# Performance work log

Hardware: AMD Instinct MI355X
Metric: run time of the kernel (lower is better)

Reference implementation:

```python
import jax, jax.numpy as jnp
import numpy as np

DIM = 2048      # model dim
H = 32          # num_heads
N = 128         # state_dim
G = 1           # num_groups
K = 4           # conv_size
HID = 4096     # hidden_dim = multiple_of*ceil(2.0*DIM/256)
P = HID // H    # head_dim = 128
CHUNK = 256
EPS = 1e-6
DT_MIN, DT_MAX = 0.001, 0.1


def setup_inputs() -> dict:
    key = jax.random.key(0)
    ks = jax.random.split(key, 8)
    b, s = 2, 2048
    d_in = 2 * HID + 2 * G * N + H           # 8448
    conv_dim = HID + 2 * G * N               # 4352
    return {
        "x": jax.random.normal(ks[0], (b, s, DIM), jnp.float32),
        "W_in": jax.random.normal(ks[1], (d_in, DIM), jnp.float32) / np.sqrt(DIM),
        "conv_w": jax.random.normal(ks[2], (conv_dim, K), jnp.float32) / np.sqrt(K),
        "conv_b": jnp.zeros((conv_dim,), jnp.float32),
        "dt_bias": jnp.zeros((H,), jnp.float32),
        "A_log": jnp.log(jax.random.uniform(ks[3], (H,), jnp.float32, 1.0, 16.0)),
        "D": jnp.ones((H,), jnp.float32),
        "norm_w": jnp.ones((HID,), jnp.float32),
        "W_out": jax.random.normal(ks[4], (DIM, HID), jnp.float32) / np.sqrt(HID),
    }


def _causal_conv_silu(xBC, w, bias):
    # depthwise causal conv1d, kernel K, then SiLU. xBC: (b,s,c), w: (c,K)
    b, s, c = xBC.shape
    xp = jnp.pad(xBC, ((0, 0), (K - 1, 0), (0, 0)))
    y = sum(xp[:, k:k + s, :] * w[:, k] for k in range(K)) + bias
    return jax.nn.silu(y)


def _chunked_scan(x, dt, A, B, C, D):
    # Mamba2 chunked selective scan.
    # x:(b,s,h,p) dt:(b,s,h) A:(h,) B,C:(b,s,n) (groups=1) D:(h,)
    b, s, h, p = x.shape
    n = B.shape[-1]
    nc, L = s // CHUNK, CHUNK
    xc = x.reshape(b, nc, L, h, p)
    dtc = dt.reshape(b, nc, L, h)
    Bc = B.reshape(b, nc, L, n)
    Cc = C.reshape(b, nc, L, n)

    dA = dtc * A                          # (b,nc,L,h), A<0
    dA_cs = jnp.cumsum(dA, axis=2)        # (b,nc,L,h)

    # intra-chunk contribution
    seg = dA_cs[:, :, :, None, :] - dA_cs[:, :, None, :, :]   # (b,nc,L,L,h)
    mask = jnp.tril(jnp.ones((L, L), bool))[None, None, :, :, None]
    decay = jnp.exp(jnp.where(mask, seg, -jnp.inf))
    CB = jnp.einsum('bcln,bcsn->bcls', Cc, Bc)                # (b,nc,L,L)
    y_intra = jnp.einsum('bcls,bclsh,bcsh,bcshp->bclhp', CB, decay, dtc, xc)

    # per-chunk final states
    decay_states = jnp.exp(dA_cs[:, :, -1:, :] - dA_cs)       # (b,nc,L,h)
    states = jnp.einsum('bclh,bclh,bclhp,bcln->bchpn', decay_states, dtc, xc, Bc)

    # inter-chunk recurrence over chunk index
    dA_chunk = dA_cs[:, :, -1, :]                              # (b,nc,h)
    def step(prev, inp):
        st, dec = inp
        new = prev * jnp.exp(dec)[:, :, None, None] + st
        return new, prev
    init = jnp.zeros((b, h, p, n), x.dtype)
    _, prev_states = jax.lax.scan(step, init,
                                  (jnp.moveaxis(states, 1, 0), jnp.moveaxis(dA_chunk, 1, 0)))
    prev_states = jnp.moveaxis(prev_states, 0, 1)              # state at start of each chunk

    y_inter = jnp.einsum('bcln,bclh,bchpn->bclhp', Cc, jnp.exp(dA_cs), prev_states)
    y = (y_intra + y_inter).reshape(b, s, h, p)
    return y + x * D[None, None, :, None]


def reference(x, W_in, conv_w, conv_b, dt_bias, A_log, D, norm_w, W_out):
    b, s, _ = x.shape
    zxbcdt = x @ W_in.T                                        # (b,s,2*HID+2GN+H)
    z, xBC, dt = jnp.split(zxbcdt, [HID, 2 * HID + 2 * G * N], axis=-1)
    xBC = _causal_conv_silu(xBC, conv_w, conv_b)
    xs, B, C = jnp.split(xBC, [HID, HID + G * N], axis=-1)
    A = -jnp.exp(A_log)
    dt = jnp.clip(jax.nn.softplus(dt + dt_bias), DT_MIN, DT_MAX)
    xs = xs.reshape(b, s, H, P)
    y = _chunked_scan(xs, dt, A, B, C, D).reshape(b, s, HID)
    y = y * jax.nn.silu(z)                                     # gate, norm_before_gate=False
    y = y * jax.lax.rsqrt(jnp.mean(y * y, axis=-1, keepdims=True) + EPS) * norm_w
    return y @ W_out.T
```

## Files before the change

### kernel.cpp

```cpp
#include <hip/hip_runtime.h>


typedef short s16x8 __attribute__((ext_vector_type(8)));
typedef float f32x4 __attribute__((ext_vector_type(4)));

__device__ __forceinline__ float bf2f(ushort u) {
    return __builtin_bit_cast(float, (unsigned)u << 16);
}
__device__ __forceinline__ ushort f2bf(float f) {
    unsigned u = __builtin_bit_cast(unsigned, f);
    unsigned r = u + 0x7fffu + ((u >> 16) & 1u);
    return (ushort)(r >> 16);
}

__device__ __forceinline__ void gld16(const void* g, void* l) {
    __builtin_amdgcn_global_load_lds((__attribute__((address_space(1))) void*)g,
                                     (__attribute__((address_space(3))) void*)l, 16, 0, 0);
}

#define BARRIER() asm volatile("s_barrier" ::: "memory")

__global__ void cast_all_k(const float4* __restrict__ x, const float4* __restrict__ wout,
                           const float4* __restrict__ win, ushort* __restrict__ xb,
                           ushort* __restrict__ woutb, ushort* __restrict__ winb) {
    const long b = blockIdx.x, tid = threadIdx.x;
    if (b < 8192) {
        long i = b * 256 + tid;
        float4 v = x[i];
        ushort4 o = { f2bf(v.x), f2bf(v.y), f2bf(v.z), f2bf(v.w) };
        *(ushort4*)(xb + i * 4) = o;
    } else if (b < 16384) {
        long i = (b - 8192) * 256 + tid;
        float4 v = wout[i];
        ushort4 o = { f2bf(v.x), f2bf(v.y), f2bf(v.z), f2bf(v.w) };
        *(ushort4*)(woutb + i * 4) = o;
    } else {
        long i = (b - 16384) * 256 + tid;
        ushort4 o;
        if (i < 4341760L) {
            float4 v = win[i];
            o = { f2bf(v.x), f2bf(v.y), f2bf(v.z), f2bf(v.w) };
        } else {
            o = { 0, 0, 0, 0 };
        }
        *(ushort4*)(winb + i * 4) = o;
    }
}

__global__ __launch_bounds__(512) void gemm1_k(const ushort* __restrict__ A,
                                               const ushort* __restrict__ Bm,
                                               ushort* __restrict__ zbuf,
                                               ushort* __restrict__ xbc,
                                               ushort* __restrict__ dtr) {
    constexpr int K = 2048, NT = 64;
    __shared__ ushort lds[2 * 8192 + 2 * 6144];
    const int tid = threadIdx.x, lane = tid & 63, wave = tid >> 6;
    const int wm = wave >> 2, wn = wave & 3;
    const int bid = blockIdx.x;
    const int xcd = bid & 7, w = bid >> 3;
    const int mt = xcd * 2 + (w & 1), nt = w >> 1;
    const long m0 = (long)mt * 256, n0 = (long)nt * 192;

    const int st_row = lane >> 2;
    const int st_gc = ((lane & 3) * 8) ^ (((lane >> 5) & 1) << 4);

    auto STAGE = [&](int buf, int kt) {
#pragma unroll
        for (int j = 0; j < 2; j++) {
            int sidx = wave + j * 8;
            gld16(A + (m0 + sidx * 16 + st_row) * K + kt + st_gc,
                  lds + buf * 8192 + sidx * 512 + lane * 8);
        }
#pragma unroll
        for (int j = 0; j < 2; j++) {
            int sidx = wave + j * 8;
            if (sidx < 12)
                gld16(Bm + (n0 + sidx * 16 + st_row) * K + kt + st_gc,
                      lds + 16384 + buf * 6144 + sidx * 512 + lane * 8);
        }
    };

    const int cfr = (lane >> 4) * 8;
    const int lr = lane & 15;
    auto LDFA = [&](int buf, int r) -> s16x8 {
        int off = buf * 8192 + ((r >> 4) << 9) + ((r & 15) << 5)
                + (cfr ^ (((r >> 3) & 1) << 4));
        return *(const s16x8*)(lds + off);
    };
    auto LDFB = [&](int buf, int r) -> s16x8 {
        int off = 16384 + buf * 6144 + ((r >> 4) << 9) + ((r & 15) << 5)
                + (cfr ^ (((r >> 3) & 1) << 4));
        return *(const s16x8*)(lds + off);
    };

    f32x4 zero = { 0.f, 0.f, 0.f, 0.f };
    f32x4 acc[8][3];
#pragma unroll
    for (int i = 0; i < 8; i++)
#pragma unroll
        for (int j = 0; j < 3; j++) acc[i][j] = zero;

    STAGE(0, 0);
    asm volatile("s_waitcnt vmcnt(0)" ::: "memory");
    BARRIER();

    for (int t = 0; t < NT; ++t) {
        const int cur = t & 1;
        if ((t + 1) < NT) STAGE((t + 1) & 1, (t + 1) * 32);

        s16x8 bfr[3], alo[4], ahi[4];
#pragma unroll
        for (int ni = 0; ni < 3; ni++) bfr[ni] = LDFB(cur, wn * 48 + ni * 16 + lr);
#pragma unroll
        for (int mi = 0; mi < 4; mi++) alo[mi] = LDFA(cur, wm * 128 + mi * 16 + lr);
#pragma unroll
        for (int mi = 0; mi < 4; mi++) ahi[mi] = LDFA(cur, wm * 128 + 64 + mi * 16 + lr);

        __builtin_amdgcn_s_setprio(1);
#pragma unroll
        for (int mi = 0; mi < 4; mi++)
#pragma unroll
            for (int ni = 0; ni < 3; ni++)
                acc[mi][ni] = __builtin_amdgcn_mfma_f32_16x16x32_bf16(alo[mi], bfr[ni], acc[mi][ni], 0, 0, 0);
#pragma unroll
        for (int mi = 0; mi < 4; mi++)
#pragma unroll
            for (int ni = 0; ni < 3; ni++)
                acc[mi + 4][ni] = __builtin_amdgcn_mfma_f32_16x16x32_bf16(ahi[mi], bfr[ni], acc[mi + 4][ni], 0, 0, 0);
        __builtin_amdgcn_s_setprio(0);

        asm volatile("s_waitcnt vmcnt(0)" ::: "memory");
        BARRIER();
    }

    const int lr4 = (lane >> 4) * 4;
#pragma unroll
    for (int mi = 0; mi < 8; mi++) {
#pragma unroll
        for (int ni = 0; ni < 3; ni++) {
            const long col = n0 + wn * 48 + ni * 16 + lr;
            ushort* dst;
            long stride;
            if (col < 4096)      { dst = zbuf + col;         stride = 4096; }
            else if (col < 8448) { dst = xbc + (col - 4096); stride = 4352; }
            else if (col < 8480) { dst = dtr + (col - 8448); stride = 32;   }
            else continue;
            const long row0 = m0 + wm * 128 + mi * 16 + lr4;
#pragma unroll
            for (int r = 0; r < 4; r++) dst[(row0 + r) * stride] = f2bf(acc[mi][ni][r]);
        }
    }
}

__global__ __launch_bounds__(256) void gemm2_k(const ushort* __restrict__ A,
                                               const ushort* __restrict__ Bm,
                                               float* __restrict__ Cout) {
    constexpr int K = 4096, NT = 128;
    __shared__ ushort lds[2 * 4096 + 2 * 4096];
    const int tid = threadIdx.x, lane = tid & 63, wave = tid >> 6;
    const int wm = wave >> 1, wn = wave & 1;
    const int bid = blockIdx.x;
    const int xcd = bid & 7, w = bid >> 3;
    const int mt = xcd * 4 + (w & 3), nt = w >> 2;
    const long m0 = (long)mt * 128, n0 = (long)nt * 128;

    const int st_row = lane >> 2;
    const int st_gc = ((lane & 3) * 8) ^ (((lane >> 5) & 1) << 4);

    auto STAGE = [&](int buf, int kt) {
#pragma unroll
        for (int j = 0; j < 2; j++) {
            int sidx = wave + j * 4;
            gld16(A + (m0 + sidx * 16 + st_row) * K + kt + st_gc,
                  lds + buf * 4096 + sidx * 512 + lane * 8);
        }
#pragma unroll
        for (int j = 0; j < 2; j++) {
            int sidx = wave + j * 4;
            gld16(Bm + (n0 + sidx * 16 + st_row) * K + kt + st_gc,
                  lds + 8192 + buf * 4096 + sidx * 512 + lane * 8);
        }
    };

    const int cfr = (lane >> 4) * 8;
    const int lr = lane & 15;
    auto LDFA = [&](int buf, int r) -> s16x8 {
        int off = buf * 4096 + ((r >> 4) << 9) + ((r & 15) << 5)
                + (cfr ^ (((r >> 3) & 1) << 4));
        return *(const s16x8*)(lds + off);
    };
    auto LDFB = [&](int buf, int r) -> s16x8 {
        int off = 8192 + buf * 4096 + ((r >> 4) << 9) + ((r & 15) << 5)
                + (cfr ^ (((r >> 3) & 1) << 4));
        return *(const s16x8*)(lds + off);
    };

    f32x4 zero = { 0.f, 0.f, 0.f, 0.f };
    f32x4 acc[4][4];
#pragma unroll
    for (int i = 0; i < 4; i++)
#pragma unroll
        for (int j = 0; j < 4; j++) acc[i][j] = zero;

    STAGE(0, 0);
    asm volatile("s_waitcnt vmcnt(0)" ::: "memory");
    BARRIER();

    for (int t = 0; t < NT; ++t) {
        const int cur = t & 1;
        if ((t + 1) < NT) STAGE((t + 1) & 1, (t + 1) * 32);

        s16x8 af[4], bf[4];
#pragma unroll
        for (int mi = 0; mi < 4; mi++) af[mi] = LDFA(cur, wm * 64 + mi * 16 + lr);
#pragma unroll
        for (int ni = 0; ni < 4; ni++) bf[ni] = LDFB(cur, wn * 64 + ni * 16 + lr);

        __builtin_amdgcn_s_setprio(1);
#pragma unroll
        for (int mi = 0; mi < 4; mi++)
#pragma unroll
            for (int ni = 0; ni < 4; ni++)
                acc[mi][ni] = __builtin_amdgcn_mfma_f32_16x16x32_bf16(af[mi], bf[ni], acc[mi][ni], 0, 0, 0);
        __builtin_amdgcn_s_setprio(0);

        asm volatile("s_waitcnt vmcnt(0)" ::: "memory");
        BARRIER();
    }

    const long crow = m0 + wm * 64 + ((lane >> 4) << 2);
    const long ccol = n0 + wn * 64 + (lane & 15);
#pragma unroll
    for (int mi = 0; mi < 4; mi++)
#pragma unroll
        for (int ni = 0; ni < 4; ni++)
#pragma unroll
            for (int r = 0; r < 4; r++)
                Cout[(crow + mi * 16 + r) * 2048 + ccol + ni * 16] = acc[mi][ni][r];
}

__global__ __launch_bounds__(256) void convx_k(const ushort* __restrict__ xbc,
                                               const float* __restrict__ w,
                                               const float* __restrict__ bias,
                                               ushort* __restrict__ xbcc,
                                               ushort* __restrict__ xT,
                                               ushort* __restrict__ Bt) {
    __shared__ ushort xin[35][136];
    __shared__ ushort yL[32][132];
    const int stile = blockIdx.x, slot = blockIdx.y, bc = blockIdx.z;
    const int tid = threadIdx.x;
    const int cc = bc & 7;
    const long tbase = (long)bc * 256 + stile * 32;
    const int c0 = slot * 128;
    const bool head = (cc == 0 && stile == 0);

#pragma unroll
    for (int i = 0; i < 3; i++) {
        int u = tid + i * 256;
        if (u < 560) {
            int r = u >> 4, seg = u & 15;
            s16x8 v;
            if (head && r < 3) {
#pragma unroll
                for (int j = 0; j < 8; j++) v[j] = 0;
            } else {
                v = *(const s16x8*)&xbc[(tbase - 3 + r) * 4352 + c0 + seg * 8];
            }
            *(s16x8*)&xin[r][seg * 8] = v;
        }
    }
    __syncthreads();

    const int s_loc = tid >> 3, p0 = (tid & 7) * 16;
    ushort yo[16];
#pragma unroll
    for (int j = 0; j < 16; j++) {
        int c = p0 + j;
        float a = bias[c0 + c];
#pragma unroll
        for (int k = 0; k < 4; k++)
            a += bf2f(xin[s_loc + k][c]) * w[(c0 + c) * 4 + k];
        float yv = a / (1.f + __expf(-a));
        ushort ub = f2bf(yv);
        yo[j] = ub;
        yL[s_loc][c] = ub;
    }
    *(s16x8*)&xbcc[(tbase + s_loc) * 4352 + c0 + p0] = *(const s16x8*)&yo[0];
    *(s16x8*)&xbcc[(tbase + s_loc) * 4352 + c0 + p0 + 8] = *(const s16x8*)&yo[8];
    __syncthreads();

    if (slot < 33) {
        const int p = tid >> 1, s0 = (tid & 1) * 16;
        ushort o[16];
#pragma unroll
        for (int j = 0; j < 16; j++) o[j] = yL[s0 + j][p];
        ushort* dst = (slot < 32)
            ? (xT + ((long)(bc * 32 + slot) * 128 + p) * 256 + stile * 32 + s0)
            : (Bt + ((long)bc * 128 + p) * 256 + stile * 32 + s0);
        *(s16x8*)&dst[0] = *(const s16x8*)&o[0];
        *(s16x8*)&dst[8] = *(const s16x8*)&o[8];
    }
}

__global__ void prep_k(const ushort* __restrict__ dtr, const float* __restrict__ dt_bias,
                       const float* __restrict__ A_log, float* __restrict__ dtp,
                       float* __restrict__ dacs) {
    const int bx = blockIdx.x;
    const int h = bx & 31, cc = (bx >> 5) & 7, bi = bx >> 8;
    const int lane = threadIdx.x;
    const float A = -__expf(A_log[h]);
    const float bsh = dt_bias[h];
    float v[4], cs[4];
    float run = 0.f;
#pragma unroll
    for (int j = 0; j < 4; j++) {
        int pos = cc * 256 + lane * 4 + j;
        float raw = bf2f(dtr[((long)(bi * 2048 + pos)) * 32 + h]) + bsh;
        float sp = (raw > 20.f) ? raw : log1pf(__expf(raw));
        float d = fminf(fmaxf(sp, 0.001f), 0.1f);
        v[j] = d;
        run += d * A;
        cs[j] = run;
    }
    float tot = run, pre = run;
    for (int off = 1; off < 64; off <<= 1) {
        float u = __shfl_up(pre, off, 64);
        if (lane >= off) pre += u;
    }
    float excl = pre - tot;
    const long base = ((long)(bi * 32 + h)) * 2048 + cc * 256 + lane * 4;
#pragma unroll
    for (int j = 0; j < 4; j++) { dtp[base + j] = v[j]; dacs[base + j] = excl + cs[j]; }
}

__global__ __launch_bounds__(256) void cb_mfma_k(const ushort* __restrict__ xbcc,
                                                 float* __restrict__ CB) {
    const int bid = blockIdx.x;
    const int sq = bid & 1, lq = (bid >> 1) & 1, bc = bid >> 2;
    const int tid = threadIdx.x, lane = tid & 63, wave = tid >> 6;
    const int wm = wave >> 1, wn = wave & 1;
    const long tbase = (long)bc * 256;

    f32x4 zero = { 0.f, 0.f, 0.f, 0.f };
    f32x4 acc[4][4];
#pragma unroll
    for (int i = 0; i < 4; i++)
#pragma unroll
        for (int j = 0; j < 4; j++) acc[i][j] = zero;

    for (int kst = 0; kst < 4; ++kst) {
        const int koff = kst * 32 + (lane >> 4) * 8;
        s16x8 a[4], b[4];
#pragma unroll
        for (int mi = 0; mi < 4; mi++) {
            int l = lq * 128 + wm * 64 + mi * 16 + (lane & 15);
            a[mi] = *(const s16x8*)&xbcc[(tbase + l) * 4352 + 4224 + koff];
        }
#pragma unroll
        for (int ni = 0; ni < 4; ni++) {
            int s = sq * 128 + wn * 64 + ni * 16 + (lane & 15);
            b[ni] = *(const s16x8*)&xbcc[(tbase + s) * 4352 + 4096 + koff];
        }
#pragma unroll
        for (int mi = 0; mi < 4; mi++)
#pragma unroll
            for (int ni = 0; ni < 4; ni++)
                acc[mi][ni] = __builtin_amdgcn_mfma_f32_16x16x32_bf16(a[mi], b[ni], acc[mi][ni], 0, 0, 0);
    }

    float* out = CB + (long)bc * 65536;
#pragma unroll
    for (int mi = 0; mi < 4; mi++)
#pragma unroll
        for (int ni = 0; ni < 4; ni++)
#pragma unroll
            for (int r = 0; r < 4; r++) {
                int l = lq * 128 + wm * 64 + mi * 16 + (lane >> 4) * 4 + r;
                int s = sq * 128 + wn * 64 + ni * 16 + (lane & 15);
                out[(long)l * 256 + s] = acc[mi][ni][r];
            }
}

__global__ __launch_bounds__(256) void scan_mfma_k(const ushort* __restrict__ xT,
                                                   const float* __restrict__ CB,
                                                   const float* __restrict__ dtp,
                                                   const float* __restrict__ dacs,
                                                   const ushort* __restrict__ xbcc,
                                                   const float* __restrict__ st,
                                                   float* __restrict__ yf) {
    const int bx = blockIdx.x;
    const int ltile = bx & 1, h = (bx >> 1) & 31, cc = (bx >> 6) & 7, bi = bx >> 9;
    const int tid = threadIdx.x, lane = tid & 63, wave = tid >> 6;
    const int wm = wave >> 1, wn = wave & 1;

    __shared__ float dA_s[256];
    __shared__ float F_s[256];

    const long dbase = ((long)(bi * 32 + h)) * 2048 + cc * 256;
    {
        float a = dacs[dbase + tid];
        float r = dacs[dbase + (tid | 31)];
        dA_s[tid] = a;
        F_s[tid] = __expf(r - a) * dtp[dbase + tid];
    }
    __syncthreads();

    int lch[4];
    float dAl[4];
#pragma unroll
    for (int mi = 0; mi < 4; mi++) {
        lch[mi] = ltile * 128 + wm * 64 + mi * 16 + (lane & 15);
        dAl[mi] = dA_s[lch[mi]];
    }

    f32x4 zero = { 0.f, 0.f, 0.f, 0.f };
    f32x4 acc[4][4];
#pragma unroll
    for (int i = 0; i < 4; i++)
#pragma unroll
        for (int j = 0; j < 4; j++) acc[i][j] = zero;

    const long tbase = (long)bi * 2048 + cc * 256;
    const long cbbase = ((long)(bi * 8 + cc)) * 65536;
    const ushort* xrow = xT + (((long)(bi * 8 + cc) * 32 + h) * 128) * 256;
    const int nsb = ltile * 4 + 4;

    for (int sb = 0; sb < nsb; ++sb) {
        const int soff = sb * 32 + (lane >> 4) * 8;
        s16x8 bf[4];
#pragma unroll
        for (int ni = 0; ni < 4; ni++) {
            int p = wn * 64 + ni * 16 + (lane & 15);
            bf[ni] = *(const s16x8*)&xrow[(long)p * 256 + soff];
        }
        const float Rsb = dA_s[sb * 32 + 31];
        const int s0 = soff;
#pragma unroll
        for (int mi = 0; mi < 4; mi++) {
            const int lb = lch[mi] >> 5;
            if (sb > lb) continue;
            const float* cbrow = CB + cbbase + (long)lch[mi] * 256 + s0;
            float4 c0 = *(const float4*)cbrow;
            float4 c1 = *(const float4*)(cbrow + 4);
            float E = __expf(dAl[mi] - Rsb);
            float m[8];
            m[0] = c0.x * E * F_s[s0 + 0]; m[1] = c0.y * E * F_s[s0 + 1];
            m[2] = c0.z * E * F_s[s0 + 2]; m[3] = c0.w * E * F_s[s0 + 3];
            m[4] = c1.x * E * F_s[s0 + 4]; m[5] = c1.y * E * F_s[s0 + 5];
            m[6] = c1.z * E * F_s[s0 + 6]; m[7] = c1.w * E * F_s[s0 + 7];
            if (sb == lb) {
#pragma unroll
                for (int j = 0; j < 8; j++)
                    if (s0 + j > lch[mi]) m[j] = 0.f;
            }
            s16x8 a;
#pragma unroll
            for (int j = 0; j < 8; j++) a[j] = (short)f2bf(m[j]);
#pragma unroll
            for (int ni = 0; ni < 4; ni++)
                acc[mi][ni] = __builtin_amdgcn_mfma_f32_16x16x32_bf16(a, bf[ni], acc[mi][ni], 0, 0, 0);
        }
    }

    const float* sbase = st + (((long)(bi * 8 + cc) * 32 + h) * 128) * 128;
    float eAr[4];
#pragma unroll
    for (int mi = 0; mi < 4; mi++) eAr[mi] = __expf(dAl[mi]);
    for (int kk = 0; kk < 4; ++kk) {
        const int koff = kk * 32 + (lane >> 4) * 8;
        s16x8 a[4], b[4];
#pragma unroll
        for (int mi = 0; mi < 4; mi++) {
            s16x8 raw = *(const s16x8*)&xbcc[(tbase + lch[mi]) * 4352 + 4224 + koff];
#pragma unroll
            for (int j = 0; j < 8; j++)
                a[mi][j] = (short)f2bf(bf2f((ushort)raw[j]) * eAr[mi]);
        }
#pragma unroll
        for (int ni = 0; ni < 4; ni++) {
            int p = wn * 64 + ni * 16 + (lane & 15);
            const float* pr = sbase + (long)p * 128 + koff;
            float4 v0 = *(const float4*)pr;
            float4 v1 = *(const float4*)(pr + 4);
            b[ni][0] = (short)f2bf(v0.x); b[ni][1] = (short)f2bf(v0.y);
            b[ni][2] = (short)f2bf(v0.z); b[ni][3] = (short)f2bf(v0.w);
            b[ni][4] = (short)f2bf(v1.x); b[ni][5] = (short)f2bf(v1.y);
            b[ni][6] = (short)f2bf(v1.z); b[ni][7] = (short)f2bf(v1.w);
        }
#pragma unroll
        for (int mi = 0; mi < 4; mi++)
#pragma unroll
            for (int ni = 0; ni < 4; ni++)
                acc[mi][ni] = __builtin_amdgcn_mfma_f32_16x16x32_bf16(a[mi], b[ni], acc[mi][ni], 0, 0, 0);
    }

    const long crow = tbase + ltile * 128 + wm * 64 + ((lane >> 4) << 2);
    const int ccol = h * 128 + wn * 64 + (lane & 15);
#pragma unroll
    for (int mi = 0; mi < 4; mi++)
#pragma unroll
        for (int ni = 0; ni < 4; ni++)
#pragma unroll
            for (int r = 0; r < 4; r++)
                yf[(crow + mi * 16 + r) * 4096 + ccol + ni * 16] = acc[mi][ni][r];
}

__global__ __launch_bounds__(256) void states_mfma_k(const ushort* __restrict__ xT,
                                                     const ushort* __restrict__ Bt,
                                                     const float* __restrict__ dtp,
                                                     const float* __restrict__ dacs,
                                                     float* __restrict__ states) {
    const int bx = blockIdx.x;
    const int h = bx & 31, cc = (bx >> 5) & 7, bi = bx >> 8;
    const int bc = bi * 8 + cc;
    const int tid = threadIdx.x, lane = tid & 63, wave = tid >> 6;
    const int wm = wave >> 1, wn = wave & 1;
    __shared__ float wl[256];
    const long dbase = ((long)(bi * 32 + h)) * 2048 + cc * 256;
    {
        float last = dacs[dbase + 255];
        wl[tid] = __expf(last - dacs[dbase + tid]) * dtp[dbase + tid];
    }
    __syncthreads();

    f32x4 zero = { 0.f, 0.f, 0.f, 0.f };
    f32x4 acc[4][4];
#pragma unroll
    for (int i = 0; i < 4; i++)
#pragma unroll
        for (int j = 0; j < 4; j++) acc[i][j] = zero;

    const ushort* xrow = xT + (((long)bc * 32 + h) * 128) * 256;
    const ushort* brow = Bt + ((long)bc * 128) * 256;

    for (int sb = 0; sb < 8; ++sb) {
        const int soff = sb * 32 + (lane >> 4) * 8;
        s16x8 a[4], b[4];
#pragma unroll
        for (int mi = 0; mi < 4; mi++) {
            int p = wm * 64 + mi * 16 + (lane & 15);
            s16x8 raw = *(const s16x8*)&xrow[(long)p * 256 + soff];
#pragma unroll
            for (int j = 0; j < 8; j++)
                a[mi][j] = (short)f2bf(bf2f((ushort)raw[j]) * wl[soff + j]);
        }
#pragma unroll
        for (int ni = 0; ni < 4; ni++) {
            int n = wn * 64 + ni * 16 + (lane & 15);
            b[ni] = *(const s16x8*)&brow[(long)n * 256 + soff];
        }
#pragma unroll
        for (int mi = 0; mi < 4; mi++)
#pragma unroll
            for (int ni = 0; ni < 4; ni++)
                acc[mi][ni] = __builtin_amdgcn_mfma_f32_16x16x32_bf16(a[mi], b[ni], acc[mi][ni], 0, 0, 0);
    }

    float* out = states + (((long)bc * 32 + h) * 128) * 128;
#pragma unroll
    for (int mi = 0; mi < 4; mi++)
#pragma unroll
        for (int ni = 0; ni < 4; ni++)
#pragma unroll
            for (int r = 0; r < 4; r++) {
                int p = wm * 64 + mi * 16 + (lane >> 4) * 4 + r;
                int n = wn * 64 + ni * 16 + (lane & 15);
                out[(long)p * 128 + n] = acc[mi][ni][r];
            }
}

__global__ void rec_k(float* __restrict__ states, const float* __restrict__ dacs) {
    const int i = blockIdx.x * 256 + threadIdx.x;
    const int n = i & 127, p = (i >> 7) & 127, h = (i >> 14) & 31, bi = i >> 19;
    const long dbase = ((long)(bi * 32 + h)) * 2048;
    float run = 0.f;
    for (int cc = 0; cc < 8; cc++) {
        const long off = ((((long)(bi * 8 + cc)) * 32 + h) * 128 + p) * 128 + n;
        float st = states[off];
        states[off] = run;
        float dec = dacs[dbase + cc * 256 + 255];
        run = run * __expf(dec) + st;
    }
}

__global__ __launch_bounds__(256) void gate_rms_k(const float* __restrict__ y, const ushort* __restrict__ zbuf,
                                                  const ushort* __restrict__ xbcc, const float* __restrict__ Dv,
                                                  const float* __restrict__ norm_w, ushort* __restrict__ yb) {
    const int t = blockIdx.x, tid = threadIdx.x;
    const float* yr = &y[(long)t * 4096];
    const ushort* zr = &zbuf[(long)t * 4096];
    const ushort* xr = &xbcc[(long)t * 4352];
    float g[16];
    float ss = 0.f;
#pragma unroll
    for (int j = 0; j < 16; j++) {
        int i = j * 256 + tid;
        float z = bf2f(zr[i]);
        float yv = yr[i] + Dv[i >> 7] * bf2f(xr[i]);
        float gv = yv * (z / (1.f + __expf(-z)));
        g[j] = gv;
        ss += gv * gv;
    }
#pragma unroll
    for (int off = 32; off > 0; off >>= 1) ss += __shfl_xor(ss, off, 64);
    __shared__ float red[4];
    if ((tid & 63) == 0) red[tid >> 6] = ss;
    __syncthreads();
    float tot = red[0] + red[1] + red[2] + red[3];
    float sc = rsqrtf(tot * (1.f / 4096.f) + 1e-6f);
#pragma unroll
    for (int j = 0; j < 16; j++) {
        int i = j * 256 + tid;
        yb[(long)t * 4096 + i] = f2bf(g[j] * sc * norm_w[i]);
    }
}

extern "C" void kernel_launch(void* const* d_in, const int* in_sizes, int n_in,
                              void* d_out, int out_size, void* d_ws, size_t ws_size,
                              hipStream_t stream) {
    const float* x       = (const float*)d_in[0];
    const float* W_in    = (const float*)d_in[1];
    const float* conv_w  = (const float*)d_in[2];
    const float* conv_b  = (const float*)d_in[3];
    const float* dt_bias = (const float*)d_in[4];
    const float* A_log   = (const float*)d_in[5];
    const float* Dv      = (const float*)d_in[6];
    const float* norm_w  = (const float*)d_in[7];
    const float* W_out   = (const float*)d_in[8];

    char* w8 = (char*)d_ws;
    ushort* xb    = (ushort*)(w8 + 0L);
    ushort* xT    = (ushort*)(w8 + 0L);
    ushort* yb    = (ushort*)(w8 + 0L);
    ushort* woutb = (ushort*)(w8 + 33554432L);
    ushort* Bt    = (ushort*)(w8 + 50331648L);
    ushort* zbuf  = (ushort*)(w8 + 52428800L);
    ushort* xbc   = (ushort*)(w8 + 85983232L);
    ushort* dtr   = (ushort*)(w8 + 121634816L);
    ushort* xbcc  = (ushort*)(w8 + 121896960L);
    float*  dtp   = (float*)(w8 + 157548544L);
    float*  dacs  = (float*)(w8 + 158072832L);
    float*  cb    = (float*)(w8 + 158597120L);
    float*  yf    = (float*)(w8 + 162791424L);
    ushort* winb  = (ushort*)(w8 + 162791424L);
    float*  st    = (float*)(w8 + 229900288L);

    cast_all_k<<<34048, 256, 0, stream>>>((const float4*)x, (const float4*)W_out,
                                          (const float4*)W_in, xb, woutb, winb);
    gemm1_k<<<736, 512, 0, stream>>>(xb, winb, zbuf, xbc, dtr);
    convx_k<<<dim3(8, 34, 16), 256, 0, stream>>>(xbc, conv_w, conv_b, xbcc, xT, Bt);
    prep_k<<<512, 64, 0, stream>>>(dtr, dt_bias, A_log, dtp, dacs);
    cb_mfma_k<<<64, 256, 0, stream>>>(xbcc, cb);
    states_mfma_k<<<512, 256, 0, stream>>>(xT, Bt, dtp, dacs, st);
    rec_k<<<4096, 256, 0, stream>>>(st, dacs);
    scan_mfma_k<<<1024, 256, 0, stream>>>(xT, cb, dtp, dacs, xbcc, st, yf);
    gate_rms_k<<<4096, 256, 0, stream>>>(yf, zbuf, xbcc, Dv, norm_w, yb);
    gemm2_k<<<512, 256, 0, stream>>>(yb, woutb, (float*)d_out);
}
```

Before: 473.9 us.

## Triple-buffer gemm1 LDS pipeline and store scan output as bf16

The input-projection GEMM moves from double to triple buffering in LDS. Tiles are prefetched two iterations ahead, and the code waits with vmcnt(3) instead of draining all loads every step, so global loads overlap more with MFMA work. Separately, the scan kernel writes its output as bf16 instead of fp32, which halves the traffic between the scan and the gate/RMSNorm kernel. The costs are more LDS per block (occupancy is pinned at one block) and a small precision loss before the norm.

```diff
diff --git a/kernel.cpp b/kernel.cpp
--- a/kernel.cpp
+++ b/kernel.cpp
@@ -47,13 +47,13 @@
     }
 }
 
-__global__ __launch_bounds__(512) void gemm1_k(const ushort* __restrict__ A,
-                                               const ushort* __restrict__ Bm,
-                                               ushort* __restrict__ zbuf,
-                                               ushort* __restrict__ xbc,
-                                               ushort* __restrict__ dtr) {
+__global__ __launch_bounds__(512, 1) void gemm1_k(const ushort* __restrict__ A,
+                                                  const ushort* __restrict__ Bm,
+                                                  ushort* __restrict__ zbuf,
+                                                  ushort* __restrict__ xbc,
+                                                  ushort* __restrict__ dtr) {
     constexpr int K = 2048, NT = 64;
-    __shared__ ushort lds[2 * 8192 + 2 * 6144];
+    __shared__ ushort lds[3 * 8192 + 3 * 6144];
     const int tid = threadIdx.x, lane = tid & 63, wave = tid >> 6;
     const int wm = wave >> 2, wn = wave & 3;
     const int bid = blockIdx.x;
@@ -64,19 +64,21 @@
     const int st_row = lane >> 2;
     const int st_gc = ((lane & 3) * 8) ^ (((lane >> 5) & 1) << 4);
 
-    auto STAGE = [&](int buf, int kt) {
+    auto STAGE_A = [&](int buf, int kt) {
 #pragma unroll
         for (int j = 0; j < 2; j++) {
             int sidx = wave + j * 8;
             gld16(A + (m0 + sidx * 16 + st_row) * K + kt + st_gc,
                   lds + buf * 8192 + sidx * 512 + lane * 8);
         }
+    };
+    auto STAGE_B = [&](int buf, int kt) {
 #pragma unroll
         for (int j = 0; j < 2; j++) {
             int sidx = wave + j * 8;
             if (sidx < 12)
                 gld16(Bm + (n0 + sidx * 16 + st_row) * K + kt + st_gc,
-                      lds + 16384 + buf * 6144 + sidx * 512 + lane * 8);
+                      lds + 24576 + buf * 6144 + sidx * 512 + lane * 8);
         }
     };
 
@@ -88,7 +90,7 @@
         return *(const s16x8*)(lds + off);
     };
     auto LDFB = [&](int buf, int r) -> s16x8 {
-        int off = 16384 + buf * 6144 + ((r >> 4) << 9) + ((r & 15) << 5)
+        int off = 24576 + buf * 6144 + ((r >> 4) << 9) + ((r & 15) << 5)
                 + (cfr ^ (((r >> 3) & 1) << 4));
         return *(const s16x8*)(lds + off);
     };
@@ -100,13 +102,16 @@
 #pragma unroll
         for (int j = 0; j < 3; j++) acc[i][j] = zero;
 
-    STAGE(0, 0);
-    asm volatile("s_waitcnt vmcnt(0)" ::: "memory");
+    STAGE_A(0, 0);  STAGE_B(0, 0);
+    STAGE_A(1, 32); STAGE_B(1, 32);
+    asm volatile("s_waitcnt vmcnt(3)" ::: "memory");
     BARRIER();
 
     for (int t = 0; t < NT; ++t) {
-        const int cur = t & 1;
-        if ((t + 1) < NT) STAGE((t + 1) & 1, (t + 1) * 32);
+        const int cur = t % 3;
+        const int nxt = (t + 2) % 3;
+        const int kt2 = (t + 2) * 32;
+        const bool do_stage = (t + 2) < NT;
 
         s16x8 bfr[3], alo[4], ahi[4];
 #pragma unroll
@@ -115,6 +120,7 @@
         for (int mi = 0; mi < 4; mi++) alo[mi] = LDFA(cur, wm * 128 + mi * 16 + lr);
 #pragma unroll
         for (int mi = 0; mi < 4; mi++) ahi[mi] = LDFA(cur, wm * 128 + 64 + mi * 16 + lr);
+        if (do_stage) { STAGE_A(nxt, kt2); STAGE_B(nxt, kt2); }
 
         __builtin_amdgcn_s_setprio(1);
 #pragma unroll
@@ -129,7 +135,8 @@
                 acc[mi + 4][ni] = __builtin_amdgcn_mfma_f32_16x16x32_bf16(ahi[mi], bfr[ni], acc[mi + 4][ni], 0, 0, 0);
         __builtin_amdgcn_s_setprio(0);
 
-        asm volatile("s_waitcnt vmcnt(0)" ::: "memory");
+        if (do_stage) asm volatile("s_waitcnt vmcnt(3)" ::: "memory");
+        else          asm volatile("s_waitcnt vmcnt(0)" ::: "memory");
         BARRIER();
     }
 
@@ -387,7 +394,7 @@
                                                    const float* __restrict__ dacs,
                                                    const ushort* __restrict__ xbcc,
                                                    const float* __restrict__ st,
-                                                   float* __restrict__ yf) {
+                                                   ushort* __restrict__ yh) {
     const int bx = blockIdx.x;
     const int ltile = bx & 1, h = (bx >> 1) & 31, cc = (bx >> 6) & 7, bi = bx >> 9;
     const int tid = threadIdx.x, lane = tid & 63, wave = tid >> 6;
@@ -502,7 +509,7 @@
         for (int ni = 0; ni < 4; ni++)
 #pragma unroll
             for (int r = 0; r < 4; r++)
-                yf[(crow + mi * 16 + r) * 4096 + ccol + ni * 16] = acc[mi][ni][r];
+                yh[(crow + mi * 16 + r) * 4096 + ccol + ni * 16] = f2bf(acc[mi][ni][r]);
 }
 
 __global__ __launch_bounds__(256) void states_mfma_k(const ushort* __restrict__ xT,
@@ -583,11 +590,11 @@
     }
 }
 
-__global__ __launch_bounds__(256) void gate_rms_k(const float* __restrict__ y, const ushort* __restrict__ zbuf,
+__global__ __launch_bounds__(256) void gate_rms_k(const ushort* __restrict__ yh, const ushort* __restrict__ zbuf,
                                                   const ushort* __restrict__ xbcc, const float* __restrict__ Dv,
                                                   const float* __restrict__ norm_w, ushort* __restrict__ yb) {
     const int t = blockIdx.x, tid = threadIdx.x;
-    const float* yr = &y[(long)t * 4096];
+    const ushort* yr = &yh[(long)t * 4096];
     const ushort* zr = &zbuf[(long)t * 4096];
     const ushort* xr = &xbcc[(long)t * 4352];
     float g[16];
@@ -596,7 +603,7 @@
     for (int j = 0; j < 16; j++) {
         int i = j * 256 + tid;
         float z = bf2f(zr[i]);
-        float yv = yr[i] + Dv[i >> 7] * bf2f(xr[i]);
+        float yv = bf2f(yr[i]) + Dv[i >> 7] * bf2f(xr[i]);
         float gv = yv * (z / (1.f + __expf(-z)));
         g[j] = gv;
         ss += gv * gv;
@@ -641,7 +648,7 @@
     float*  dtp   = (float*)(w8 + 157548544L);
     float*  dacs  = (float*)(w8 + 158072832L);
     float*  cb    = (float*)(w8 + 158597120L);
-    float*  yf    = (float*)(w8 + 162791424L);
+    ushort* yh    = (ushort*)(w8 + 162791424L);
     ushort* winb  = (ushort*)(w8 + 162791424L);
     float*  st    = (float*)(w8 + 229900288L);
 
@@ -653,7 +660,7 @@
     cb_mfma_k<<<64, 256, 0, stream>>>(xbcc, cb);
     states_mfma_k<<<512, 256, 0, stream>>>(xT, Bt, dtp, dacs, st);
     rec_k<<<4096, 256, 0, stream>>>(st, dacs);
-    scan_mfma_k<<<1024, 256, 0, stream>>>(xT, cb, dtp, dacs, xbcc, st, yf);
-    gate_rms_k<<<4096, 256, 0, stream>>>(yf, zbuf, xbcc, Dv, norm_w, yb);
+    scan_mfma_k<<<1024, 256, 0, stream>>>(xT, cb, dtp, dacs, xbcc, st, yh);
+    gate_rms_k<<<4096, 256, 0, stream>>>(yh, zbuf, xbcc, Dv, norm_w, yb);
     gemm2_k<<<512, 256, 0, stream>>>(yb, woutb, (float*)d_out);
 }
```

Result: faster. 459.3 us (-3.1%).
